# Kernel optimization log

Measured on AMD Instinct MI355X. Metric: run time of the kernel, lower is better.

Reference implementation:

```python
import jax, jax.numpy as jnp
import numpy as np

SIZE = 20          # nodes per graph instance ('size' expert index)
NUM_CLONE = 2000   # number of cloned graphs in the batch
H = 128            # hidden_dim
L = 3              # num_layers (depth)
N = SIZE * NUM_CLONE
E = NUM_CLONE * SIZE * (SIZE - 1)  # complete digraph per clone
EPS = 1e-5


def _edge_index_np():
    ii, jj = np.meshgrid(np.arange(SIZE), np.arange(SIZE), indexing='ij')
    m = ii != jj
    s, d = ii[m], jj[m]                      # [380] local src/dst
    off = (np.arange(NUM_CLONE) * SIZE)[:, None]
    src = (s[None, :] + off).reshape(-1)
    dst = (d[None, :] + off).reshape(-1)
    return np.stack([src, dst]).astype(np.int32)


def setup_inputs() -> dict:
    key = jax.random.key(0)
    ks = jax.random.split(key, 16)
    s_h = 1.0 / np.sqrt(H)
    s_f = 1.0 / np.sqrt(4 * H)
    inp = {
        'x': jax.random.normal(ks[0], (N, H), jnp.float32),
        'edge_attr': jax.random.normal(ks[1], (E, H), jnp.float32),
        # ResGatedGraphConv params (Linear weights stored as [in, out], bias=False)
        'Wk': jax.random.normal(ks[2], (L, H, H), jnp.float32) * s_h,
        'Wq': jax.random.normal(ks[3], (L, H, H), jnp.float32) * s_h,
        'Wv': jax.random.normal(ks[4], (L, H, H), jnp.float32) * s_h,
        'We': jax.random.normal(ks[5], (L, H, H), jnp.float32) * s_h,
        'Wskip': jax.random.normal(ks[6], (L, H, H), jnp.float32) * s_h,
        # FFN_Expert params (Expert-20), no bias
        'W1': jax.random.normal(ks[7], (L, H, 4 * H), jnp.float32) * s_h,
        'W2': jax.random.normal(ks[8], (L, 4 * H, H), jnp.float32) * s_f,
        # LayerNorm affine params (bias=True)
        'g1': jnp.ones((L, H), jnp.float32),
        'b1': jnp.zeros((L, H), jnp.float32),
        'g2': jnp.ones((L, H), jnp.float32),
        'b2': jnp.zeros((L, H), jnp.float32),
        'edge_index': jnp.asarray(_edge_index_np()),
        'size': SIZE,
    }
    return inp


def _layer_norm(x, g, b):
    mu = jnp.mean(x, axis=-1, keepdims=True)
    var = jnp.mean(jnp.square(x - mu), axis=-1, keepdims=True)
    return (x - mu) * jax.lax.rsqrt(var + EPS) * g + b


def reference(x, edge_attr, Wk, Wq, Wv, We, Wskip, W1, W2, g1, b1, g2, b2, edge_index, size):
    # ConvNetwork: stacked ConvLayer(ResGatedGraph) blocks; dropout=0 (eval)
    src, dst = edge_index[0], edge_index[1]
    n = x.shape[0]
    h = x
    for l in range(L):
        k = h @ Wk[l]                 # [N,H] keys (target role)
        q = h @ Wq[l]                 # [N,H] queries (source role)
        v = h @ Wv[l]                 # [N,H] values (source role)
        e = edge_attr @ We[l]         # [E,H] edge-conditioned term
        gate = jax.nn.sigmoid(k[dst] + q[src] + e)      # [E,H]
        msg = gate * v[src]                              # [E,H]
        agg = jax.ops.segment_sum(msg, dst, num_segments=n)  # scatter-add
        out = agg + h @ Wskip[l]      # skip / root weight
        out = _layer_norm(out, g1[l], b1[l])             # norm1
        # per-size FFN expert (Expert-<size>): Linear->GELU(exact)->Linear
        ffn = jax.nn.gelu(out @ W1[l], approximate=False) @ W2[l]
        h = _layer_norm(out + ffn, g2[l], b2[l])         # norm2
    return h
```

## Files before the change

kernel.cpp:

```cpp
#include <hip/hip_runtime.h>
#include <math.h>

#define NSIZE 20
#define NC 2000
#define H 128
#define NLAYER 3
#define EPB 380
#define NGRP 20

typedef float f32x4 __attribute__((ext_vector_type(4)));
typedef unsigned int u32x4 __attribute__((ext_vector_type(4)));
typedef unsigned short us8 __attribute__((ext_vector_type(8)));
typedef __bf16 bf16x8 __attribute__((ext_vector_type(8)));
typedef unsigned long long u64;

#define OW_E 0
#define OW_K 2048
#define OW_Q 4096
#define OW_V 6144
#define OW_S 8192
#define OW_1 10240
#define OW_2 18432
#define OW_LAYER 26624
#define EA_OFF_B 2097152
#define EA_ELEMS 97280000
#define WS_NEED (EA_OFF_B + (size_t)EA_ELEMS*2)

#define L_HBF   0
#define L_X2    8704
#define L_QARR  8704
#define L_VARR  14304
#define L_BM    25600
#define L_TOT   36160

static __device__ __forceinline__ unsigned short f2bf(float f){
  unsigned u = __float_as_uint(f);
  u += 0x7fffu + ((u >> 16) & 1u);
  return (unsigned short)(u >> 16);
}
static __device__ __forceinline__ float bf2f(unsigned short b){
  return __uint_as_float(((unsigned)b) << 16);
}
static __device__ __forceinline__ unsigned pkbf(float a, float b){
  return (unsigned)f2bf(a) | ((unsigned)f2bf(b) << 16);
}
static __device__ __forceinline__ f32x4 MFMA(u32x4 a, u32x4 b, f32x4 c){
  return __builtin_amdgcn_mfma_f32_16x16x32_bf16(
      __builtin_bit_cast(bf16x8, a), __builtin_bit_cast(bf16x8, b), c, 0, 0, 0);
}
static __device__ __forceinline__ float sigm(float x){
  return __builtin_amdgcn_rcpf(1.f + __expf(-x));
}

__global__ __launch_bounds__(256) void pack_weights(
    const float* __restrict__ Wk, const float* __restrict__ Wq,
    const float* __restrict__ Wv, const float* __restrict__ We,
    const float* __restrict__ Ws, const float* __restrict__ W1,
    const float* __restrict__ W2, u32x4* __restrict__ outp)
{
  int l = blockIdx.x / 7, m = blockIdx.x % 7;
  const float* src; int K, N; long base;
  switch(m){
    case 0: src = We + (long)l*H*H;   K=H;   N=H;   base=OW_E; break;
    case 1: src = Wk + (long)l*H*H;   K=H;   N=H;   base=OW_K; break;
    case 2: src = Wq + (long)l*H*H;   K=H;   N=H;   base=OW_Q; break;
    case 3: src = Wv + (long)l*H*H;   K=H;   N=H;   base=OW_V; break;
    case 4: src = Ws + (long)l*H*H;   K=H;   N=H;   base=OW_S; break;
    case 5: src = W1 + (long)l*H*4*H; K=H;   N=4*H; base=OW_1; break;
    default: src = W2 + (long)l*4*H*H; K=4*H; N=H;  base=OW_2; break;
  }
  base += (long)l * OW_LAYER;
  int KT = K/32, NT = N/16;
  int total = KT*NT*64;
  for(int i = threadIdx.x; i < total; i += 256){
    int lane = i & 63, f = i >> 6;
    int kt = f % KT, nt = f / KT;
    int col = nt*16 + (lane & 15);
    int k0 = kt*32 + (lane >> 4)*8;
    us8 v;
    #pragma unroll
    for(int j=0;j<8;++j) v[j] = f2bf(src[(long)(k0+j)*N + col]);
    outp[base + (long)f*64 + lane] = __builtin_bit_cast(u32x4, v);
  }
}

template<bool EAB>
__global__ __launch_bounds__(256, 4) void moe_gnn(
    const float* __restrict__ x, const float* __restrict__ ea,
    unsigned short* __restrict__ eab,
    const float* __restrict__ g1, const float* __restrict__ b1,
    const float* __restrict__ g2, const float* __restrict__ b2,
    const u32x4* __restrict__ wp, float* __restrict__ out)
{
  __shared__ __align__(16) unsigned char smem[L_TOT];
  unsigned short* hbf  = (unsigned short*)(smem + L_HBF);
  unsigned short* x2   = (unsigned short*)(smem + L_X2);
  unsigned short* qarr = (unsigned short*)(smem + L_QARR);
  unsigned short* varr = (unsigned short*)(smem + L_VARR);
  float*          Bm   = (float*)(smem + L_BM);

  const int c   = blockIdx.x;
  const int tid = threadIdx.x;
  const int w   = tid >> 6;
  const int l   = tid & 63;
  const int lg  = l >> 4;
  const int l15 = l & 15;
  const long cEPB = (long)c * EPB;

  if(EAB){
    const f32x4* src = (const f32x4*)(ea + cEPB*H);
    u32x4* dst = (u32x4*)(eab + cEPB*H);
    for(int i = tid; i < EPB*H/8; i += 256){
      f32x4 a = src[2*i], b = src[2*i+1];
      dst[i] = (u32x4){ pkbf(a[0],a[1]), pkbf(a[2],a[3]),
                        pkbf(b[0],b[1]), pkbf(b[2],b[3]) };
    }
  }
  for(int i = tid; i < 32*H; i += 256){
    int r = i >> 7, cc = i & 127;
    float v = (r < NSIZE) ? x[((long)c*NSIZE + r)*H + cc] : 0.f;
    hbf[r*136 + cc] = f2bf(v);
  }
  __syncthreads();

  #pragma unroll 1
  for(int layer = 0; layer < NLAYER; ++layer){
    const u32x4* wl = wp + (long)layer*OW_LAYER;
    f32x4 kreg[2][2];
    f32x4 agg[2][2];

    {
      u32x4 hb[2][4];
      #pragma unroll
      for(int nt=0; nt<2; ++nt)
        #pragma unroll
        for(int kt=0; kt<4; ++kt)
          hb[nt][kt] = *(const u32x4*)&hbf[(nt*16+l15)*136 + kt*32 + lg*8];

      #pragma unroll
      for(int m=0; m<4; ++m){
        const long ow = (m==0?OW_K: m==1?OW_Q: m==2?OW_V: OW_S);
        #pragma unroll
        for(int mt=0; mt<2; ++mt)
          #pragma unroll
          for(int nt=0; nt<2; ++nt){
            f32x4 acc = {0.f,0.f,0.f,0.f};
            #pragma unroll
            for(int kt=0; kt<4; ++kt)
              acc = MFMA(wl[ow + (((2*w+mt)*4)+kt)*64 + l], hb[nt][kt], acc);
            if(m==0) kreg[mt][nt] = acc;
            else if(m==3) agg[mt][nt] = acc;
            else {
              unsigned short* dst = (m==1) ? qarr : varr;
              if(nt==0 || l15 < 4){
                u64 pk = (u64)pkbf(acc[0],acc[1]) | ((u64)pkbf(acc[2],acc[3]) << 32);
                *(u64*)&dst[(nt*16+l15)*140 + (2*w+mt)*16 + lg*4] = pk;
              }
            }
          }
      }
    }

    {
      u32x4 eB[2][4];
      #pragma unroll
      for(int mt=0;mt<2;++mt)
        #pragma unroll
        for(int kt=0;kt<4;++kt)
          eB[mt][kt] = wl[OW_E + ((2*w+mt)*4+kt)*64 + l];

      #pragma unroll 2
      for(int g=0; g<NGRP; ++g){
        bool va = (l15 != g);
        int s = l15 - ((l15 > g) ? 1 : 0);
        long row = cEPB + (long)g*19 + (va ? s : 0);
        u32x4 ef[4];
        if(EAB){
          const unsigned short* ep = eab + row*H + lg*8;
          #pragma unroll
          for(int kt=0;kt<4;++kt) ef[kt] = *(const u32x4*)(ep + kt*32);
        } else {
          const float* ap = ea + row*H + lg*8;
          #pragma unroll
          for(int kt=0;kt<4;++kt){
            f32x4 lo = *(const f32x4*)(ap + kt*32);
            f32x4 hi = *(const f32x4*)(ap + kt*32 + 4);
            ef[kt] = (u32x4){ pkbf(lo[0],lo[1]), pkbf(lo[2],lo[3]),
                              pkbf(hi[0],hi[1]), pkbf(hi[2],hi[3]) };
          }
        }
        #pragma unroll
        for(int mt=0; mt<2; ++mt){
          u64 q8 = *(const u64*)&qarr[g*140 + (2*w+mt)*16 + lg*4];
          u64 v8 = *(const u64*)&varr[g*140 + (2*w+mt)*16 + lg*4];
          f32x4 acc = {0.f,0.f,0.f,0.f};
          #pragma unroll
          for(int kt=0;kt<4;++kt)
            acc = MFMA(eB[mt][kt], ef[kt], acc);
          #pragma unroll
          for(int j=0;j<4;++j){
            float q_ = bf2f((unsigned short)(q8 >> (16*j)));
            float v_ = bf2f((unsigned short)(v8 >> (16*j)));
            float xg = acc[j] + kreg[mt][0][j] + q_;
            float m_ = sigm(xg) * v_;
            agg[mt][0][j] += va ? m_ : 0.f;
          }
        }
      }

      {
        const int qi = l15 >> 2, di = l15 & 3;
        f32x4 aggR[2];
        aggR[0] = (f32x4){0.f,0.f,0.f,0.f};
        aggR[1] = (f32x4){0.f,0.f,0.f,0.f};
        #pragma unroll 1
        for(int qb=0; qb<NGRP; qb+=4){
          int g = qb + qi;
          int d = 16 + di;
          bool va = (d != g);
          int s = d - ((d > g) ? 1 : 0);
          long row = cEPB + (long)g*19 + (va ? s : 0);
          u32x4 ef[4];
          if(EAB){
            const unsigned short* ep = eab + row*H + lg*8;
            #pragma unroll
            for(int kt=0;kt<4;++kt) ef[kt] = *(const u32x4*)(ep + kt*32);
          } else {
            const float* ap = ea + row*H + lg*8;
            #pragma unroll
            for(int kt=0;kt<4;++kt){
              f32x4 lo = *(const f32x4*)(ap + kt*32);
              f32x4 hi = *(const f32x4*)(ap + kt*32 + 4);
              ef[kt] = (u32x4){ pkbf(lo[0],lo[1]), pkbf(lo[2],lo[3]),
                                pkbf(hi[0],hi[1]), pkbf(hi[2],hi[3]) };
            }
          }
          #pragma unroll
          for(int mt=0; mt<2; ++mt){
            u64 q8 = *(const u64*)&qarr[g*140 + (2*w+mt)*16 + lg*4];
            u64 v8 = *(const u64*)&varr[g*140 + (2*w+mt)*16 + lg*4];
            f32x4 acc = {0.f,0.f,0.f,0.f};
            #pragma unroll
            for(int kt=0;kt<4;++kt)
              acc = MFMA(eB[mt][kt], ef[kt], acc);
            #pragma unroll
            for(int j=0;j<4;++j){
              float kk = __shfl(kreg[mt][1][j], (lg<<4) | di, 64);
              float q_ = bf2f((unsigned short)(q8 >> (16*j)));
              float v_ = bf2f((unsigned short)(v8 >> (16*j)));
              float xg = acc[j] + kk + q_;
              float m_ = sigm(xg) * v_;
              aggR[mt][j] += va ? m_ : 0.f;
            }
          }
        }
        #pragma unroll
        for(int mt=0; mt<2; ++mt)
          #pragma unroll
          for(int j=0;j<4;++j){
            float t = aggR[mt][j];
            t += __shfl_xor(t, 4, 64);
            t += __shfl_xor(t, 8, 64);
            agg[mt][1][j] += t;
          }
      }

      #pragma unroll
      for(int nt=0; nt<2; ++nt)
        if(nt==0 || l15 < 4)
          #pragma unroll
          for(int mt=0; mt<2; ++mt)
            *(f32x4*)&Bm[(nt*16+l15)*132 + (2*w+mt)*16 + lg*4] = agg[mt][nt];
    }
    __syncthreads();

    {
      const float* gp = g1 + layer*H; const float* bp = b1 + layer*H;
      float gv0 = gp[l], gv1 = gp[64+l], bv0 = bp[l], bv1 = bp[64+l];
      for(int i=0;i<5;++i){
        int r = w + 4*i;
        float v0 = Bm[r*132 + l], v1 = Bm[r*132 + 64 + l];
        float s = v0+v1;
        #pragma unroll
        for(int m=1;m<64;m<<=1) s += __shfl_xor(s, m, 64);
        float mu = s*(1.f/128.f);
        float d0=v0-mu, d1=v1-mu;
        float qv = d0*d0 + d1*d1;
        #pragma unroll
        for(int m=1;m<64;m<<=1) qv += __shfl_xor(qv, m, 64);
        float rs = rsqrtf(qv*(1.f/128.f) + 1e-5f);
        float y0 = d0*rs*gv0 + bv0;
        float y1 = d1*rs*gv1 + bv1;
        Bm[r*132 + l] = y0; Bm[r*132 + 64 + l] = y1;
        hbf[r*136 + l] = f2bf(y0); hbf[r*136 + 64 + l] = f2bf(y1);
      }
    }
    __syncthreads();

    {
      u32x4 hb2[2][4];
      #pragma unroll
      for(int nt=0;nt<2;++nt)
        #pragma unroll
        for(int kt=0;kt<4;++kt)
          hb2[nt][kt] = *(const u32x4*)&hbf[(nt*16+l15)*136 + kt*32 + lg*8];
      f32x4 c2[2][2];
      #pragma unroll
      for(int mt=0;mt<2;++mt)
        #pragma unroll
        for(int nt=0;nt<2;++nt)
          c2[mt][nt] = (f32x4){0.f,0.f,0.f,0.f};
      #pragma unroll 1
      for(int hh=0; hh<2; ++hh){
        for(int i2=0;i2<4;++i2){
          int mtg = hh*16 + w*4 + i2;
          #pragma unroll
          for(int nt=0;nt<2;++nt){
            f32x4 acc = {0.f,0.f,0.f,0.f};
            #pragma unroll
            for(int kt=0;kt<4;++kt)
              acc = MFMA(wl[OW_1 + (mtg*4+kt)*64 + l], hb2[nt][kt], acc);
            float ge[4];
            #pragma unroll
            for(int j=0;j<4;++j){
              float v = acc[j];
              float u = v*(0.7978845608f + 0.0356774081f*v*v);
              ge[j] = v * sigm(2.f*u);
            }
            u64 pk = (u64)pkbf(ge[0],ge[1]) | ((u64)pkbf(ge[2],ge[3]) << 32);
            *(u64*)&x2[(nt*16+l15)*264 + (w*4+i2)*16 + lg*4] = pk;
          }
        }
        __syncthreads();
        #pragma unroll
        for(int nt=0;nt<2;++nt){
          #pragma unroll
          for(int kt=0;kt<8;++kt){
            u32x4 xb = *(const u32x4*)&x2[(nt*16+l15)*264 + kt*32 + lg*8];
            #pragma unroll
            for(int mt=0;mt<2;++mt)
              c2[mt][nt] = MFMA(wl[OW_2 + ((2*w+mt)*16 + hh*8 + kt)*64 + l],
                                xb, c2[mt][nt]);
          }
        }
        __syncthreads();
      }
      #pragma unroll
      for(int nt=0;nt<2;++nt)
        if(nt==0 || l15 < 4)
          #pragma unroll
          for(int mt=0;mt<2;++mt){
            float* p = &Bm[(nt*16+l15)*132 + (2*w+mt)*16 + lg*4];
            *(f32x4*)p = *(f32x4*)p + c2[mt][nt];
          }
    }
    __syncthreads();

    {
      const float* gp = g2 + layer*H; const float* bp = b2 + layer*H;
      float gv0 = gp[l], gv1 = gp[64+l], bv0 = bp[l], bv1 = bp[64+l];
      for(int i=0;i<5;++i){
        int r = w + 4*i;
        float v0 = Bm[r*132 + l], v1 = Bm[r*132 + 64 + l];
        float s = v0+v1;
        #pragma unroll
        for(int m=1;m<64;m<<=1) s += __shfl_xor(s, m, 64);
        float mu = s*(1.f/128.f);
        float d0=v0-mu, d1=v1-mu;
        float qv = d0*d0 + d1*d1;
        #pragma unroll
        for(int m=1;m<64;m<<=1) qv += __shfl_xor(qv, m, 64);
        float rs = rsqrtf(qv*(1.f/128.f) + 1e-5f);
        float y0 = d0*rs*gv0 + bv0;
        float y1 = d1*rs*gv1 + bv1;
        hbf[r*136 + l] = f2bf(y0); hbf[r*136 + 64 + l] = f2bf(y1);
        if(layer == NLAYER-1){
          out[((long)c*NSIZE + r)*H + l]      = y0;
          out[((long)c*NSIZE + r)*H + 64 + l] = y1;
        }
      }
    }
    __syncthreads();
  }
}

extern "C" void kernel_launch(void* const* d_in, const int* in_sizes, int n_in,
                              void* d_out, int out_size, void* d_ws, size_t ws_size,
                              hipStream_t stream) {
  const float* x  = (const float*)d_in[0];
  const float* ea = (const float*)d_in[1];
  const float* Wk = (const float*)d_in[2];
  const float* Wq = (const float*)d_in[3];
  const float* Wv = (const float*)d_in[4];
  const float* We = (const float*)d_in[5];
  const float* Ws = (const float*)d_in[6];
  const float* W1 = (const float*)d_in[7];
  const float* W2 = (const float*)d_in[8];
  const float* g1 = (const float*)d_in[9];
  const float* b1 = (const float*)d_in[10];
  const float* g2 = (const float*)d_in[11];
  const float* b2 = (const float*)d_in[12];
  u32x4* wp = (u32x4*)d_ws;

  hipLaunchKernelGGL(pack_weights, dim3(21), dim3(256), 0, stream,
                     Wk, Wq, Wv, We, Ws, W1, W2, wp);
  if(ws_size >= WS_NEED){
    unsigned short* eab = (unsigned short*)((char*)d_ws + EA_OFF_B);
    hipLaunchKernelGGL(moe_gnn<true>, dim3(NC), dim3(256), 0, stream,
                       x, ea, eab, g1, b1, g2, b2, wp, (float*)d_out);
  } else {
    hipLaunchKernelGGL(moe_gnn<false>, dim3(NC), dim3(256), 0, stream,
                       x, ea, (unsigned short*)nullptr,
                       g1, b1, g2, b2, wp, (float*)d_out);
  }
}
```

Measured before the change: 604.0 us.

## Shrink shared memory by aliasing buffers and storing residuals in bf16

Cuts per-block LDS from about 36KB to about 16KB. It trims the padded node rows from 32 to 20 and clamps the MFMA B-operand row index. It also aliases the q/v, x2 and accumulator buffers into one region and keeps the residual/LayerNorm staging in bf16 inside hbf instead of a separate fp32 buffer. The aim is higher occupancy, at the cost of extra rounding of pre-norm activations to bf16 and one added barrier.

```diff
diff --git a/kernel.cpp b/kernel.cpp
--- a/kernel.cpp
+++ b/kernel.cpp
@@ -27,11 +27,11 @@
 #define WS_NEED (EA_OFF_B + (size_t)EA_ELEMS*2)
 
 #define L_HBF   0
-#define L_X2    8704
-#define L_QARR  8704
-#define L_VARR  14304
-#define L_BM    25600
-#define L_TOT   36160
+#define L_QARR  5440
+#define L_VARR  11040
+#define L_X2    5440
+#define L_BM    5440
+#define L_TOT   16640
 
 static __device__ __forceinline__ unsigned short f2bf(float f){
   unsigned u = __float_as_uint(f);
@@ -97,7 +97,7 @@
   unsigned short* x2   = (unsigned short*)(smem + L_X2);
   unsigned short* qarr = (unsigned short*)(smem + L_QARR);
   unsigned short* varr = (unsigned short*)(smem + L_VARR);
-  float*          Bm   = (float*)(smem + L_BM);
+  unsigned short* Bm   = (unsigned short*)(smem + L_BM);
 
   const int c   = blockIdx.x;
   const int tid = threadIdx.x;
@@ -106,6 +106,7 @@
   const int lg  = l >> 4;
   const int l15 = l & 15;
   const long cEPB = (long)c * EPB;
+  const int rown[2] = { l15, (16 + l15 > 19) ? 19 : 16 + l15 };
 
   if(EAB){
     const f32x4* src = (const f32x4*)(ea + cEPB*H);
@@ -116,10 +117,9 @@
                         pkbf(b[0],b[1]), pkbf(b[2],b[3]) };
     }
   }
-  for(int i = tid; i < 32*H; i += 256){
+  for(int i = tid; i < NSIZE*H; i += 256){
     int r = i >> 7, cc = i & 127;
-    float v = (r < NSIZE) ? x[((long)c*NSIZE + r)*H + cc] : 0.f;
-    hbf[r*136 + cc] = f2bf(v);
+    hbf[r*136 + cc] = f2bf(x[((long)c*NSIZE + r)*H + cc]);
   }
   __syncthreads();
 
@@ -135,7 +135,7 @@
       for(int nt=0; nt<2; ++nt)
         #pragma unroll
         for(int kt=0; kt<4; ++kt)
-          hb[nt][kt] = *(const u32x4*)&hbf[(nt*16+l15)*136 + kt*32 + lg*8];
+          hb[nt][kt] = *(const u32x4*)&hbf[rown[nt]*136 + kt*32 + lg*8];
 
       #pragma unroll
       for(int m=0; m<4; ++m){
@@ -265,12 +265,16 @@
           }
       }
 
+      __syncthreads();
+
       #pragma unroll
       for(int nt=0; nt<2; ++nt)
         if(nt==0 || l15 < 4)
           #pragma unroll
           for(int mt=0; mt<2; ++mt)
-            *(f32x4*)&Bm[(nt*16+l15)*132 + (2*w+mt)*16 + lg*4] = agg[mt][nt];
+            *(u64*)&Bm[(nt*16+l15)*132 + (2*w+mt)*16 + lg*4] =
+              (u64)pkbf(agg[mt][nt][0], agg[mt][nt][1]) |
+              ((u64)pkbf(agg[mt][nt][2], agg[mt][nt][3]) << 32);
     }
     __syncthreads();
 
@@ -279,7 +283,7 @@
       float gv0 = gp[l], gv1 = gp[64+l], bv0 = bp[l], bv1 = bp[64+l];
       for(int i=0;i<5;++i){
         int r = w + 4*i;
-        float v0 = Bm[r*132 + l], v1 = Bm[r*132 + 64 + l];
+        float v0 = bf2f(Bm[r*132 + l]), v1 = bf2f(Bm[r*132 + 64 + l]);
         float s = v0+v1;
         #pragma unroll
         for(int m=1;m<64;m<<=1) s += __shfl_xor(s, m, 64);
@@ -291,7 +295,6 @@
         float rs = rsqrtf(qv*(1.f/128.f) + 1e-5f);
         float y0 = d0*rs*gv0 + bv0;
         float y1 = d1*rs*gv1 + bv1;
-        Bm[r*132 + l] = y0; Bm[r*132 + 64 + l] = y1;
         hbf[r*136 + l] = f2bf(y0); hbf[r*136 + 64 + l] = f2bf(y1);
       }
     }
@@ -303,7 +306,7 @@
       for(int nt=0;nt<2;++nt)
         #pragma unroll
         for(int kt=0;kt<4;++kt)
-          hb2[nt][kt] = *(const u32x4*)&hbf[(nt*16+l15)*136 + kt*32 + lg*8];
+          hb2[nt][kt] = *(const u32x4*)&hbf[rown[nt]*136 + kt*32 + lg*8];
       f32x4 c2[2][2];
       #pragma unroll
       for(int mt=0;mt<2;++mt)
@@ -327,8 +330,10 @@
               float u = v*(0.7978845608f + 0.0356774081f*v*v);
               ge[j] = v * sigm(2.f*u);
             }
-            u64 pk = (u64)pkbf(ge[0],ge[1]) | ((u64)pkbf(ge[2],ge[3]) << 32);
-            *(u64*)&x2[(nt*16+l15)*264 + (w*4+i2)*16 + lg*4] = pk;
+            if(nt==0 || l15 < 4){
+              u64 pk = (u64)pkbf(ge[0],ge[1]) | ((u64)pkbf(ge[2],ge[3]) << 32);
+              *(u64*)&x2[(nt*16+l15)*264 + (w*4+i2)*16 + lg*4] = pk;
+            }
           }
         }
         __syncthreads();
@@ -336,7 +341,7 @@
         for(int nt=0;nt<2;++nt){
           #pragma unroll
           for(int kt=0;kt<8;++kt){
-            u32x4 xb = *(const u32x4*)&x2[(nt*16+l15)*264 + kt*32 + lg*8];
+            u32x4 xb = *(const u32x4*)&x2[rown[nt]*264 + kt*32 + lg*8];
             #pragma unroll
             for(int mt=0;mt<2;++mt)
               c2[mt][nt] = MFMA(wl[OW_2 + ((2*w+mt)*16 + hh*8 + kt)*64 + l],
@@ -350,8 +355,13 @@
         if(nt==0 || l15 < 4)
           #pragma unroll
           for(int mt=0;mt<2;++mt){
-            float* p = &Bm[(nt*16+l15)*132 + (2*w+mt)*16 + lg*4];
-            *(f32x4*)p = *(f32x4*)p + c2[mt][nt];
+            unsigned short* p = &hbf[(nt*16+l15)*136 + (2*w+mt)*16 + lg*4];
+            u64 o8 = *(u64*)p;
+            float r0 = bf2f((unsigned short)(o8      )) + c2[mt][nt][0];
+            float r1 = bf2f((unsigned short)(o8 >> 16)) + c2[mt][nt][1];
+            float r2 = bf2f((unsigned short)(o8 >> 32)) + c2[mt][nt][2];
+            float r3 = bf2f((unsigned short)(o8 >> 48)) + c2[mt][nt][3];
+            *(u64*)p = (u64)pkbf(r0,r1) | ((u64)pkbf(r2,r3) << 32);
           }
     }
     __syncthreads();
@@ -361,7 +371,7 @@
       float gv0 = gp[l], gv1 = gp[64+l], bv0 = bp[l], bv1 = bp[64+l];
       for(int i=0;i<5;++i){
         int r = w + 4*i;
-        float v0 = Bm[r*132 + l], v1 = Bm[r*132 + 64 + l];
+        float v0 = bf2f(hbf[r*136 + l]), v1 = bf2f(hbf[r*136 + 64 + l]);
         float s = v0+v1;
         #pragma unroll
         for(int m=1;m<64;m<<=1) s += __shfl_xor(s, m, 64);
```

New measurement: 623.3 us. 3.2% more time.
